# Performance work log

Hardware: AMD Instinct MI355X
Metric: run time of the kernel (lower is better)

## Reference

```python
import jax, jax.numpy as jnp
from jax import lax
import numpy as np

V, E, H, B, S = 50000, 128, 64, 512, 512
OUT = 2


def _lstm_layer(x, Wih, Whh, bih, bhh):
    # x: [B, S, D]; Wih: [4H, D]; Whh: [4H, H]; PyTorch gate order i,f,g,o
    b = bih + bhh
    Bsz = x.shape[0]
    h0 = jnp.zeros((Bsz, H), x.dtype)
    c0 = jnp.zeros((Bsz, H), x.dtype)
    # precompute input projections for all timesteps (one big GEMM)
    xproj = jnp.einsum('bsd,gd->bsg', x, Wih) + b  # [B, S, 4H]

    def step(carry, xt):
        h, c = carry
        gates = xt + h @ Whh.T  # [B, 4H]
        i, f, g, o = jnp.split(gates, 4, axis=-1)
        i = jax.nn.sigmoid(i)
        f = jax.nn.sigmoid(f)
        g = jnp.tanh(g)
        o = jax.nn.sigmoid(o)
        c = f * c + i * g
        h = o * jnp.tanh(c)
        return (h, c), h

    (hT, cT), ys = lax.scan(step, (h0, c0), jnp.swapaxes(xproj, 0, 1))
    return jnp.swapaxes(ys, 0, 1), hT


def setup_inputs() -> dict:
    key = jax.random.key(0)
    ks = jax.random.split(key, 12)
    s = 0.05
    emb = jax.random.normal(ks[0], (V, E), jnp.float32) * s
    emb = emb.at[0].set(0.0)  # padding_idx=0
    inp = {
        'input_seq': jax.random.randint(ks[1], (B, S), 0, V, dtype=jnp.int64),
        'emb': emb,
        'Wih0': jax.random.normal(ks[2], (4 * H, E), jnp.float32) * s,
        'Whh0': jax.random.normal(ks[3], (4 * H, H), jnp.float32) * s,
        'bih0': jax.random.normal(ks[4], (4 * H,), jnp.float32) * s,
        'bhh0': jax.random.normal(ks[5], (4 * H,), jnp.float32) * s,
        'Wih1': jax.random.normal(ks[6], (4 * H, H), jnp.float32) * s,
        'Whh1': jax.random.normal(ks[7], (4 * H, H), jnp.float32) * s,
        'bih1': jax.random.normal(ks[8], (4 * H,), jnp.float32) * s,
        'bhh1': jax.random.normal(ks[9], (4 * H,), jnp.float32) * s,
        'Wfc': jax.random.normal(ks[10], (OUT, H), jnp.float32) * s,
        'bfc': jax.random.normal(ks[11], (OUT,), jnp.float32) * s,
    }
    return inp


def reference(input_seq, emb, Wih0, Whh0, bih0, bhh0, Wih1, Whh1, bih1, bhh1, Wfc, bfc):
    # eval-mode: dropouts are identity
    x = emb[input_seq]                       # [B, S, E] embedding lookup
    y0, h0T = _lstm_layer(x, Wih0, Whh0, bih0, bhh0)
    y1, h1T = _lstm_layer(y0, Wih1, Whh1, bih1, bhh1)
    out = jax.nn.sigmoid(h1T @ Wfc.T + bfc)  # [B, 2]
    return out
```

## Files before the change

### kernel.cpp

```cpp
#include <hip/hip_runtime.h>
#include <hip/hip_bf16.h>
#include <hip/hip_fp16.h>
#include <math.h>

#define Bv   512
#define Sv   512
#define Hv   64
#define Ev   128
#define G4   256
#define VV   50000
#define Rr   16
#define NTILE ((VV + 31) / 32)

typedef _Float16 f16;
typedef _Float16 f16x2 __attribute__((ext_vector_type(2)));
typedef _Float16 f16x4 __attribute__((ext_vector_type(4)));
typedef _Float16 f16x8 __attribute__((ext_vector_type(8)));
typedef float    f32x4 __attribute__((ext_vector_type(4)));

#if __has_builtin(__builtin_amdgcn_exp2f)
#define EXP2F(x) __builtin_amdgcn_exp2f(x)
#else
#define EXP2F(x) exp2f(x)
#endif
#if __has_builtin(__builtin_amdgcn_rcpf)
#define RCPF(x) __builtin_amdgcn_rcpf(x)
#else
#define RCPF(x) (1.0f / (x))
#endif
#define LOG2E 1.442695040888963f

#define BAR_LDS() do {                                         \
    asm volatile("s_waitcnt lgkmcnt(0)" ::: "memory");         \
    __builtin_amdgcn_s_barrier();                              \
    asm volatile("" ::: "memory");                             \
} while (0)

__device__ __forceinline__ float fast_sigmoid(float x) {
    float e = EXP2F(-LOG2E * x);
    return RCPF(1.0f + e);
}

__device__ __forceinline__ f16x2 PK(float a, float b) {
    return __builtin_bit_cast(f16x2, __builtin_amdgcn_cvt_pkrtz(a, b));
}
__device__ __forceinline__ f16x2 C2(float c) {
    f16 h = (f16)c;
    return f16x2{h, h};
}
__device__ __forceinline__ f16x2 sig2(f16x2 x) {
    f16x2 x2 = x * x;
    f16x2 t = x2 * C2(2.08333333e-3f) + C2(-2.08333333e-2f);
    t = x2 * t + C2(0.25f);
    return x * t + C2(0.5f);
}
__device__ __forceinline__ f16x2 tanh2(f16x2 x) {
    f16x2 x2 = x * x;
    f16x2 t = x2 * C2(1.33333333e-1f) + C2(-3.33333333e-1f);
    t = x2 * t + C2(1.f);
    return x * t;
}

__device__ __forceinline__ void cell_update4(const f32x4 acc[4], f16x2 c2[2],
                                             f16* dst, int stride) {
#pragma unroll
    for (int p = 0; p < 2; ++p) {
        f16x2 ig = sig2 (PK(acc[0][2 * p], acc[0][2 * p + 1]));
        f16x2 fg = sig2 (PK(acc[1][2 * p], acc[1][2 * p + 1]));
        f16x2 gg = tanh2(PK(acc[2][2 * p], acc[2][2 * p + 1]));
        f16x2 og = sig2 (PK(acc[3][2 * p], acc[3][2 * p + 1]));
        c2[p] = fg * c2[p] + ig * gg;
        f16x2 hv = og * tanh2(c2[p]);
        dst[(2 * p) * stride]     = hv[0];
        dst[(2 * p + 1) * stride] = hv[1];
    }
}

__device__ __forceinline__ f16x8 cvt8(float4 a, float4 b) {
    f16x2 p0 = PK(a.x, a.y), p1 = PK(a.z, a.w);
    f16x2 p2 = PK(b.x, b.y), p3 = PK(b.z, b.w);
    f16x8 r;
    r[0] = p0[0]; r[1] = p0[1]; r[2] = p1[0]; r[3] = p1[1];
    r[4] = p2[0]; r[5] = p2[1]; r[6] = p3[0]; r[7] = p3[1];
    return r;
}

__global__ __launch_bounds__(256) void vocab_gemm_mfma(
    const float* __restrict__ emb,
    const float* __restrict__ Wih0,
    const float* __restrict__ bih0, const float* __restrict__ bhh0,
    f16* __restrict__ P2)
{
    const int tid  = threadIdx.x;
    const int w    = tid >> 6;
    const int lane = tid & 63;
    const int col  = lane & 15;
    const int quad = lane >> 4;
    const int u    = 16 * w + col;

    __shared__ __align__(16) f16 sA[32][136];

    const size_t m0 = (size_t)blockIdx.x * 32;

    const int sr = tid >> 3;
    const int sc = (tid & 7) * 16;
    size_t rg = m0 + sr;
    if (rg >= VV) rg = 0;
    const float4* ap = (const float4*)(emb + rg * (size_t)Ev + sc);
    float4 v0 = ap[0], v1 = ap[1], v2 = ap[2], v3 = ap[3];

    f16x8 Bf[4][4];
    float bb[4];
#pragma unroll
    for (int tt = 0; tt < 4; ++tt) {
        const int n = 64 * tt + u;
#pragma unroll
        for (int kc = 0; kc < 4; ++kc) {
            const float4* bp = (const float4*)(Wih0 + (size_t)n * Ev + kc * 32 + quad * 8);
            Bf[tt][kc] = cvt8(bp[0], bp[1]);
        }
        bb[tt] = bih0[n] + bhh0[n];
    }

    *(f16x8*)&sA[sr][sc]     = cvt8(v0, v1);
    *(f16x8*)&sA[sr][sc + 8] = cvt8(v2, v3);
    __syncthreads();

    f16x8 Af[2][4];
#pragma unroll
    for (int mh = 0; mh < 2; ++mh)
#pragma unroll
        for (int kc = 0; kc < 4; ++kc)
            Af[mh][kc] = *(const f16x8*)&sA[mh * 16 + col][kc * 32 + quad * 8];

    f32x4 acc[2][4];
#pragma unroll
    for (int mh = 0; mh < 2; ++mh)
#pragma unroll
        for (int tt = 0; tt < 4; ++tt) {
#pragma unroll
            for (int r = 0; r < 4; ++r) acc[mh][tt][r] = 0.f;
#pragma unroll
            for (int kc = 0; kc < 4; ++kc)
                acc[mh][tt] = __builtin_amdgcn_mfma_f32_16x16x32_f16(
                    Af[mh][kc], Bf[tt][kc], acc[mh][tt], 0, 0, 0);
        }

#pragma unroll
    for (int mh = 0; mh < 2; ++mh)
#pragma unroll
        for (int r = 0; r < 4; ++r) {
            size_t row = m0 + mh * 16 + quad * 4 + r;
            if (row < VV) {
                f16x4 pk;
#pragma unroll
                for (int tt = 0; tt < 4; ++tt)
                    pk[tt] = (f16)(acc[mh][tt][r] + bb[tt]);
                *(f16x4*)(P2 + row * (size_t)G4 + u * 4) = pk;
            }
        }
}

__device__ __forceinline__ void load_chunk(uint2 (&X)[4][4],
    const int (*idxl)[516], int rowbase, int sb, const f16* Pl2) {
    if (sb > Sv - 4) sb = Sv - 4;
#pragma unroll
    for (int r = 0; r < 4; ++r) {
        int4 v = *(const int4*)&idxl[rowbase + r][sb];
        X[r][0] = *(const uint2*)(Pl2 + (size_t)(unsigned)v.x * G4);
        X[r][1] = *(const uint2*)(Pl2 + (size_t)(unsigned)v.y * G4);
        X[r][2] = *(const uint2*)(Pl2 + (size_t)(unsigned)v.z * G4);
        X[r][3] = *(const uint2*)(Pl2 + (size_t)(unsigned)v.w * G4);
    }
}

__global__ __launch_bounds__(512) void lstm_mfma(
    const f16* __restrict__ P2,
    const int* __restrict__ idx,
    const float* __restrict__ Whh0,
    const float* __restrict__ Wih1,
    const float* __restrict__ Whh1,
    const float* __restrict__ bih1, const float* __restrict__ bhh1,
    const float* __restrict__ Wfc,
    const float* __restrict__ bfc,
    float* __restrict__ out)
{
    const int tid  = threadIdx.x;
    const int wave = tid >> 6;
    const int lane = tid & 63;
    const int grp  = wave >> 2;
    const int w    = wave & 3;
    const int col  = lane & 15;
    const int quad = lane >> 4;
    const int u    = 16 * w + col;
    const int rowbase = quad * 4;
    const int rb   = blockIdx.x * Rr;

    __shared__ __align__(16) f16 h0b[4][Rr][72];
    __shared__ __align__(16) f16 h1b[2][Rr][72];
    __shared__ __align__(16) int idxl[Rr][516];

    for (int k = tid; k < Rr * Sv; k += 512) {
        int r = k >> 9, s = k & 511;
        idxl[r][s] = idx[(size_t)(rb + r) * Sv + s];
    }
    for (int k = tid; k < 4 * Rr * 72; k += 512)
        (&h0b[0][0][0])[k] = (f16)0.f;
    for (int k = tid; k < 2 * Rr * 72; k += 512)
        (&h1b[0][0][0])[k] = (f16)0.f;

    f16x8 Bh[4][2];
    f16x8 Bi[4][2];
    f16x8 B1[4][2];
    f32x4 bgv[4];
    if (grp == 0) {
#pragma unroll
        for (int g = 0; g < 4; ++g) {
            const int n = u + 64 * g;
#pragma unroll
            for (int kt = 0; kt < 2; ++kt) {
                const float4* sp = (const float4*)(Whh0 + (size_t)n * Hv + kt * 32 + quad * 8);
                Bh[g][kt] = cvt8(sp[0], sp[1]);
            }
        }
    } else {
#pragma unroll
        for (int g = 0; g < 4; ++g) {
            const int n = u + 64 * g;
#pragma unroll
            for (int kt = 0; kt < 2; ++kt) {
                const float4* si = (const float4*)(Wih1 + (size_t)n * Hv + kt * 32 + quad * 8);
                const float4* s1 = (const float4*)(Whh1 + (size_t)n * Hv + kt * 32 + quad * 8);
                Bi[g][kt] = cvt8(si[0], si[1]);
                B1[g][kt] = cvt8(s1[0], s1[1]);
            }
            float b = bih1[n] + bhh1[n];
            bgv[g] = f32x4{b, b, b, b};
        }
    }

    f16x2 c2[2] = {C2(0.f), C2(0.f)};
    uint2 Xa[4][4], Xb[4][4];
    f16x8 pa0[2], pa1[2];
    const f16* Pl2 = P2 + u * 4;

    __syncthreads();

    if (grp == 0) load_chunk(Xa, idxl, rowbase, 0, Pl2);

    for (int o = 0; o < Sv / 8; ++o) {
        const int s0 = o * 8;
#pragma unroll
        for (int jj = 0; jj < 8; ++jj) {
            const int i = s0 + jj;
            if (grp == 0) {
                const int rp = (i + 3) & 3;
                const int wp = i & 3;
                f32x4 acc[4];
#pragma unroll
                for (int r = 0; r < 4; ++r) {
                    f16x4 xf = __builtin_bit_cast(f16x4,
                        (jj < 4) ? Xa[r][jj & 3] : Xb[r][jj & 3]);
#pragma unroll
                    for (int g = 0; g < 4; ++g) acc[g][r] = (float)xf[g];
                }
                if (jj == 0) load_chunk(Xb, idxl, rowbase, s0 + 4, Pl2);
                if (jj == 4) load_chunk(Xa, idxl, rowbase, s0 + 8, Pl2);
                f16x8 a0 = *(const f16x8*)&h0b[rp][col][quad * 8];
                f16x8 a1 = *(const f16x8*)&h0b[rp][col][32 + quad * 8];
#pragma unroll
                for (int g = 0; g < 4; ++g) {
                    acc[g] = __builtin_amdgcn_mfma_f32_16x16x32_f16(a0, Bh[g][0], acc[g], 0, 0, 0);
                    acc[g] = __builtin_amdgcn_mfma_f32_16x16x32_f16(a1, Bh[g][1], acc[g], 0, 0, 0);
                }
                cell_update4(acc, c2, &h0b[wp][rowbase][u], 72);
            } else {
                const int pu = i & 1;
                if (i >= 2) {
                    const int rs1 = (i + 1) & 1;
                    const int ws1 = i & 1;
                    f16x8 a10 = *(const f16x8*)&h1b[rs1][col][quad * 8];
                    f16x8 a11 = *(const f16x8*)&h1b[rs1][col][32 + quad * 8];
                    {
                        const int pf = (i + 3) & 3;
                        pa0[pu ^ 1] = *(const f16x8*)&h0b[pf][col][quad * 8];
                        pa1[pu ^ 1] = *(const f16x8*)&h0b[pf][col][32 + quad * 8];
                    }
                    f32x4 acc[4];
#pragma unroll
                    for (int g = 0; g < 4; ++g) {
                        f32x4 t = __builtin_amdgcn_mfma_f32_16x16x32_f16(pa0[pu], Bi[g][0], bgv[g], 0, 0, 0);
                        t = __builtin_amdgcn_mfma_f32_16x16x32_f16(pa1[pu], Bi[g][1], t, 0, 0, 0);
                        t = __builtin_amdgcn_mfma_f32_16x16x32_f16(a10, B1[g][0], t, 0, 0, 0);
                        acc[g] = __builtin_amdgcn_mfma_f32_16x16x32_f16(a11, B1[g][1], t, 0, 0, 0);
                    }
                    cell_update4(acc, c2, &h1b[ws1][rowbase][u], 72);
                } else if (i >= 1) {
                    const int pf = (i + 3) & 3;
                    pa0[pu ^ 1] = *(const f16x8*)&h0b[pf][col][quad * 8];
                    pa1[pu ^ 1] = *(const f16x8*)&h0b[pf][col][32 + quad * 8];
                }
            }
            BAR_LDS();
        }
    }

    if (grp == 1) {
        f16x8 a10 = *(const f16x8*)&h1b[1][col][quad * 8];
        f16x8 a11 = *(const f16x8*)&h1b[1][col][32 + quad * 8];
        pa0[1] = *(const f16x8*)&h0b[3][col][quad * 8];
        pa1[1] = *(const f16x8*)&h0b[3][col][32 + quad * 8];
        f32x4 acc[4];
#pragma unroll
        for (int g = 0; g < 4; ++g) {
            f32x4 t = __builtin_amdgcn_mfma_f32_16x16x32_f16(pa0[0], Bi[g][0], bgv[g], 0, 0, 0);
            t = __builtin_amdgcn_mfma_f32_16x16x32_f16(pa1[0], Bi[g][1], t, 0, 0, 0);
            t = __builtin_amdgcn_mfma_f32_16x16x32_f16(a10, B1[g][0], t, 0, 0, 0);
            acc[g] = __builtin_amdgcn_mfma_f32_16x16x32_f16(a11, B1[g][1], t, 0, 0, 0);
        }
        cell_update4(acc, c2, &h1b[0][rowbase][u], 72);
    }
    __syncthreads();

    if (grp == 1) {
        f16x8 a10 = *(const f16x8*)&h1b[0][col][quad * 8];
        f16x8 a11 = *(const f16x8*)&h1b[0][col][32 + quad * 8];
        f32x4 acc[4];
#pragma unroll
        for (int g = 0; g < 4; ++g) {
            f32x4 t = __builtin_amdgcn_mfma_f32_16x16x32_f16(pa0[1], Bi[g][0], bgv[g], 0, 0, 0);
            t = __builtin_amdgcn_mfma_f32_16x16x32_f16(pa1[1], Bi[g][1], t, 0, 0, 0);
            t = __builtin_amdgcn_mfma_f32_16x16x32_f16(a10, B1[g][0], t, 0, 0, 0);
            acc[g] = __builtin_amdgcn_mfma_f32_16x16x32_f16(a11, B1[g][1], t, 0, 0, 0);
        }
        cell_update4(acc, c2, &h1b[1][rowbase][u], 72);
    }
    __syncthreads();

    if (tid < 2 * Rr) {
        const int r = tid >> 1, j = tid & 1;
        float s = bfc[j];
        const float* wf = Wfc + (size_t)j * Hv;
#pragma unroll 8
        for (int k = 0; k < Hv; ++k) s += (float)h1b[1][r][k] * wf[k];
        out[(size_t)(rb + r) * 2 + j] = fast_sigmoid(s);
    }
}

extern "C" void kernel_launch(void* const* d_in, const int* in_sizes, int n_in,
                              void* d_out, int out_size, void* d_ws, size_t ws_size,
                              hipStream_t stream)
{
    const int*   idx  = (const int*)  d_in[0];
    const float* emb  = (const float*)d_in[1];
    const float* Wih0 = (const float*)d_in[2];
    const float* Whh0 = (const float*)d_in[3];
    const float* bih0 = (const float*)d_in[4];
    const float* bhh0 = (const float*)d_in[5];
    const float* Wih1 = (const float*)d_in[6];
    const float* Whh1 = (const float*)d_in[7];
    const float* bih1 = (const float*)d_in[8];
    const float* bhh1 = (const float*)d_in[9];
    const float* Wfc  = (const float*)d_in[10];
    const float* bfc  = (const float*)d_in[11];
    float* out = (float*)d_out;

    f16* P2 = (f16*)d_ws;

    vocab_gemm_mfma<<<NTILE, 256, 0, stream>>>(emb, Wih0, bih0, bhh0, P2);
    lstm_mfma<<<Bv / Rr, 512, 0, stream>>>(P2, idx, Whh0,
                                           Wih1, Whh1, bih1, bhh1, Wfc, bfc, out);
}
```

Baseline: 387.6 us.

## Move layer-1 input projection to layer-0 waves and pass gates through LDS

Layer-0 waves now also compute the layer-1 input projection (Wih1·h0 plus bias) from the h0 fragments they already hold. They write the partial gates to a double-buffered LDS array, and layer-1 waves read it back, so each layer-1 step drops from four MFMA chains to two. This rebalances work between the two wave groups, which share a per-step barrier, at the cost of extra MFMA and LDS traffic on the layer-0 side. Separately, gather addressing is simplified: indices are pre-shifted by 9 and added to a 32-bit per-thread offset, replacing 64-bit multiply-add address math.

After: 414.2 us. 6.9% more time.

```diff
diff --git a/kernel.cpp b/kernel.cpp
--- a/kernel.cpp
+++ b/kernel.cpp
@@ -162,15 +162,16 @@
 }
 
 __device__ __forceinline__ void load_chunk(uint2 (&X)[4][4],
-    const int (*idxl)[516], int rowbase, int sb, const f16* Pl2) {
+    const int (*idxl)[516], int rowbase, int sb,
+    const char* __restrict__ p2b, uint32_t ulo) {
     if (sb > Sv - 4) sb = Sv - 4;
 #pragma unroll
     for (int r = 0; r < 4; ++r) {
         int4 v = *(const int4*)&idxl[rowbase + r][sb];
-        X[r][0] = *(const uint2*)(Pl2 + (size_t)(unsigned)v.x * G4);
-        X[r][1] = *(const uint2*)(Pl2 + (size_t)(unsigned)v.y * G4);
-        X[r][2] = *(const uint2*)(Pl2 + (size_t)(unsigned)v.z * G4);
-        X[r][3] = *(const uint2*)(Pl2 + (size_t)(unsigned)v.w * G4);
+        X[r][0] = *(const uint2*)(p2b + (uint32_t)((uint32_t)v.x + ulo));
+        X[r][1] = *(const uint2*)(p2b + (uint32_t)((uint32_t)v.y + ulo));
+        X[r][2] = *(const uint2*)(p2b + (uint32_t)((uint32_t)v.z + ulo));
+        X[r][3] = *(const uint2*)(p2b + (uint32_t)((uint32_t)v.w + ulo));
     }
 }
 
@@ -198,11 +199,12 @@
 
     __shared__ __align__(16) f16 h0b[4][Rr][72];
     __shared__ __align__(16) f16 h1b[2][Rr][72];
+    __shared__ __align__(16) float tgb[2][4][64][20];
     __shared__ __align__(16) int idxl[Rr][516];
 
     for (int k = tid; k < Rr * Sv; k += 512) {
         int r = k >> 9, s = k & 511;
-        idxl[r][s] = idx[(size_t)(rb + r) * Sv + s];
+        idxl[r][s] = idx[(size_t)(rb + r) * Sv + s] << 9;
     }
     for (int k = tid; k < 4 * Rr * 72; k += 512)
         (&h0b[0][0][0])[k] = (f16)0.f;
@@ -220,33 +222,33 @@
 #pragma unroll
             for (int kt = 0; kt < 2; ++kt) {
                 const float4* sp = (const float4*)(Whh0 + (size_t)n * Hv + kt * 32 + quad * 8);
+                const float4* si = (const float4*)(Wih1 + (size_t)n * Hv + kt * 32 + quad * 8);
                 Bh[g][kt] = cvt8(sp[0], sp[1]);
-            }
-        }
-    } else {
-#pragma unroll
-        for (int g = 0; g < 4; ++g) {
-            const int n = u + 64 * g;
-#pragma unroll
-            for (int kt = 0; kt < 2; ++kt) {
-                const float4* si = (const float4*)(Wih1 + (size_t)n * Hv + kt * 32 + quad * 8);
-                const float4* s1 = (const float4*)(Whh1 + (size_t)n * Hv + kt * 32 + quad * 8);
                 Bi[g][kt] = cvt8(si[0], si[1]);
-                B1[g][kt] = cvt8(s1[0], s1[1]);
             }
             float b = bih1[n] + bhh1[n];
             bgv[g] = f32x4{b, b, b, b};
         }
+    } else {
+#pragma unroll
+        for (int g = 0; g < 4; ++g) {
+            const int n = u + 64 * g;
+#pragma unroll
+            for (int kt = 0; kt < 2; ++kt) {
+                const float4* s1 = (const float4*)(Whh1 + (size_t)n * Hv + kt * 32 + quad * 8);
+                B1[g][kt] = cvt8(s1[0], s1[1]);
+            }
+        }
     }
 
     f16x2 c2[2] = {C2(0.f), C2(0.f)};
     uint2 Xa[4][4], Xb[4][4];
-    f16x8 pa0[2], pa1[2];
-    const f16* Pl2 = P2 + u * 4;
+    const char* p2b = (const char*)P2;
+    const uint32_t ulo = (uint32_t)(u * 8);
 
     __syncthreads();
 
-    if (grp == 0) load_chunk(Xa, idxl, rowbase, 0, Pl2);
+    if (grp == 0) load_chunk(Xa, idxl, rowbase, 0, p2b, ulo);
 
     for (int o = 0; o < Sv / 8; ++o) {
         const int s0 = o * 8;
@@ -264,8 +266,8 @@
 #pragma unroll
                     for (int g = 0; g < 4; ++g) acc[g][r] = (float)xf[g];
                 }
-                if (jj == 0) load_chunk(Xb, idxl, rowbase, s0 + 4, Pl2);
-                if (jj == 4) load_chunk(Xa, idxl, rowbase, s0 + 8, Pl2);
+                if (jj == 0) load_chunk(Xb, idxl, rowbase, s0 + 4, p2b, ulo);
+                if (jj == 4) load_chunk(Xa, idxl, rowbase, s0 + 8, p2b, ulo);
                 f16x8 a0 = *(const f16x8*)&h0b[rp][col][quad * 8];
                 f16x8 a1 = *(const f16x8*)&h0b[rp][col][32 + quad * 8];
 #pragma unroll
@@ -273,49 +275,50 @@
                     acc[g] = __builtin_amdgcn_mfma_f32_16x16x32_f16(a0, Bh[g][0], acc[g], 0, 0, 0);
                     acc[g] = __builtin_amdgcn_mfma_f32_16x16x32_f16(a1, Bh[g][1], acc[g], 0, 0, 0);
                 }
+                if (i >= 1) {
+#pragma unroll
+                    for (int g = 0; g < 4; ++g) {
+                        f32x4 t = __builtin_amdgcn_mfma_f32_16x16x32_f16(a0, Bi[g][0], bgv[g], 0, 0, 0);
+                        t = __builtin_amdgcn_mfma_f32_16x16x32_f16(a1, Bi[g][1], t, 0, 0, 0);
+                        *(f32x4*)&tgb[(i - 1) & 1][g][u][quad * 4] = t;
+                    }
+                }
                 cell_update4(acc, c2, &h0b[wp][rowbase][u], 72);
-            } else {
-                const int pu = i & 1;
-                if (i >= 2) {
-                    const int rs1 = (i + 1) & 1;
-                    const int ws1 = i & 1;
-                    f16x8 a10 = *(const f16x8*)&h1b[rs1][col][quad * 8];
-                    f16x8 a11 = *(const f16x8*)&h1b[rs1][col][32 + quad * 8];
-                    {
-                        const int pf = (i + 3) & 3;
-                        pa0[pu ^ 1] = *(const f16x8*)&h0b[pf][col][quad * 8];
-                        pa1[pu ^ 1] = *(const f16x8*)&h0b[pf][col][32 + quad * 8];
-                    }
-                    f32x4 acc[4];
-#pragma unroll
-                    for (int g = 0; g < 4; ++g) {
-                        f32x4 t = __builtin_amdgcn_mfma_f32_16x16x32_f16(pa0[pu], Bi[g][0], bgv[g], 0, 0, 0);
-                        t = __builtin_amdgcn_mfma_f32_16x16x32_f16(pa1[pu], Bi[g][1], t, 0, 0, 0);
-                        t = __builtin_amdgcn_mfma_f32_16x16x32_f16(a10, B1[g][0], t, 0, 0, 0);
-                        acc[g] = __builtin_amdgcn_mfma_f32_16x16x32_f16(a11, B1[g][1], t, 0, 0, 0);
-                    }
-                    cell_update4(acc, c2, &h1b[ws1][rowbase][u], 72);
-                } else if (i >= 1) {
-                    const int pf = (i + 3) & 3;
-                    pa0[pu ^ 1] = *(const f16x8*)&h0b[pf][col][quad * 8];
-                    pa1[pu ^ 1] = *(const f16x8*)&h0b[pf][col][32 + quad * 8];
+            } else if (i >= 2) {
+                const int rs1 = (i + 1) & 1;
+                const int ws1 = i & 1;
+                f16x8 a10 = *(const f16x8*)&h1b[rs1][col][quad * 8];
+                f16x8 a11 = *(const f16x8*)&h1b[rs1][col][32 + quad * 8];
+                f32x4 acc[4];
+#pragma unroll
+                for (int g = 0; g < 4; ++g) {
+                    f32x4 cs = *(const f32x4*)&tgb[i & 1][g][u][quad * 4];
+                    f32x4 t = __builtin_amdgcn_mfma_f32_16x16x32_f16(a10, B1[g][0], cs, 0, 0, 0);
+                    acc[g] = __builtin_amdgcn_mfma_f32_16x16x32_f16(a11, B1[g][1], t, 0, 0, 0);
                 }
+                cell_update4(acc, c2, &h1b[ws1][rowbase][u], 72);
             }
             BAR_LDS();
         }
     }
 
-    if (grp == 1) {
+    if (grp == 0) {
+        f16x8 a0 = *(const f16x8*)&h0b[3][col][quad * 8];
+        f16x8 a1 = *(const f16x8*)&h0b[3][col][32 + quad * 8];
+#pragma unroll
+        for (int g = 0; g < 4; ++g) {
+            f32x4 t = __builtin_amdgcn_mfma_f32_16x16x32_f16(a0, Bi[g][0], bgv[g], 0, 0, 0);
+            t = __builtin_amdgcn_mfma_f32_16x16x32_f16(a1, Bi[g][1], t, 0, 0, 0);
+            *(f32x4*)&tgb[1][g][u][quad * 4] = t;
+        }
+    } else {
         f16x8 a10 = *(const f16x8*)&h1b[1][col][quad * 8];
         f16x8 a11 = *(const f16x8*)&h1b[1][col][32 + quad * 8];
-        pa0[1] = *(const f16x8*)&h0b[3][col][quad * 8];
-        pa1[1] = *(const f16x8*)&h0b[3][col][32 + quad * 8];
         f32x4 acc[4];
 #pragma unroll
         for (int g = 0; g < 4; ++g) {
-            f32x4 t = __builtin_amdgcn_mfma_f32_16x16x32_f16(pa0[0], Bi[g][0], bgv[g], 0, 0, 0);
-            t = __builtin_amdgcn_mfma_f32_16x16x32_f16(pa1[0], Bi[g][1], t, 0, 0, 0);
-            t = __builtin_amdgcn_mfma_f32_16x16x32_f16(a10, B1[g][0], t, 0, 0, 0);
+            f32x4 cs = *(const f32x4*)&tgb[0][g][u][quad * 4];
+            f32x4 t = __builtin_amdgcn_mfma_f32_16x16x32_f16(a10, B1[g][0], cs, 0, 0, 0);
             acc[g] = __builtin_amdgcn_mfma_f32_16x16x32_f16(a11, B1[g][1], t, 0, 0, 0);
         }
         cell_update4(acc, c2, &h1b[0][rowbase][u], 72);
@@ -328,9 +331,8 @@
         f32x4 acc[4];
 #pragma unroll
         for (int g = 0; g < 4; ++g) {
-            f32x4 t = __builtin_amdgcn_mfma_f32_16x16x32_f16(pa0[1], Bi[g][0], bgv[g], 0, 0, 0);
-            t = __builtin_amdgcn_mfma_f32_16x16x32_f16(pa1[1], Bi[g][1], t, 0, 0, 0);
-            t = __builtin_amdgcn_mfma_f32_16x16x32_f16(a10, B1[g][0], t, 0, 0, 0);
+            f32x4 cs = *(const f32x4*)&tgb[1][g][u][quad * 4];
+            f32x4 t = __builtin_amdgcn_mfma_f32_16x16x32_f16(a10, B1[g][0], cs, 0, 0, 0);
             acc[g] = __builtin_amdgcn_mfma_f32_16x16x32_f16(a11, B1[g][1], t, 0, 0, 0);
         }
         cell_update4(acc, c2, &h1b[1][rowbase][u], 72);
```
